# Kernel optimization log

Measured on AMD Instinct MI355X. Metric: run time of the kernel, lower is better.

Reference implementation:

```python
import jax, jax.numpy as jnp
import numpy as np

B, I, O = 128, 256, 4096
DECAY = 0.95


def setup_inputs() -> dict:
    key = jax.random.key(0)
    k_x, k_stim, k_a = jax.random.split(key, 3)
    return {
        "x": jax.random.normal(k_x, (B, I), dtype=jnp.float32),
        "stim": jax.random.normal(k_stim, (O, I), dtype=jnp.float32),
        "a": jax.random.normal(k_a, (O,), dtype=jnp.float32),
        "b": jnp.ones((O,), dtype=jnp.float32),
        "state": jnp.zeros((B, O), dtype=jnp.float32),
    }


def reference(x, stim, a, b, state):
    # L-inf distance between every input row and every stimulus row.
    # (B, 1, I) - (1, O, I) -> (B, O, I); max over input dim -> (B, O)
    distances = jnp.max(jnp.abs(x[:, None, :] - stim[None, :, :]), axis=-1)
    value = jax.nn.sigmoid((a[None, :] - distances) * b[None, :])  # (B, O)
    new_state = state * DECAY + value
    return new_state
```

## Files before the change

kernel.cpp:

```cpp
#include <hip/hip_runtime.h>
#include <math.h>

#define BB 128
#define II 256
#define OO 4096
#define DECAY 0.95f

constexpr int TB  = 16;
constexpr int TO  = 64;
constexpr int IC  = 64;
constexpr int PAD = 4;
constexpr int LDW = IC + PAD;

__global__ __launch_bounds__(256) void stimulus_linf_kernel(
    const float* __restrict__ x,
    const float* __restrict__ stim,
    const float* __restrict__ a,
    const float* __restrict__ b,
    const float* __restrict__ state,
    float* __restrict__ out)
{
    __shared__ float s_stim[TO][LDW];

    const int tid  = threadIdx.x;
    const int lane = tid & 63;
    const int wave = tid >> 6;

    const int o_tile  = blockIdx.x & 63;
    const int bi_tile = blockIdx.x >> 6;
    const int o_base  = o_tile * TO;
    const int bi_base = bi_tile * TB;

    const int wrow = __builtin_amdgcn_readfirstlane(bi_base + wave * 4);

    float d[4] = {0.f, 0.f, 0.f, 0.f};

    for (int ic = 0; ic < II; ic += IC) {
        #pragma unroll
        for (int k = 0; k < 4; ++k) {
            const int idx = tid + k * 256;
            const int row = idx >> 4;
            const int c4  = idx & 15;
            const float4 v = *reinterpret_cast<const float4*>(
                &stim[(o_base + row) * II + ic + c4 * 4]);
            *reinterpret_cast<float4*>(&s_stim[row][c4 * 4]) = v;
        }
        __syncthreads();

        const float4* xr0 = reinterpret_cast<const float4*>(x + (wrow + 0) * II + ic);
        const float4* xr1 = reinterpret_cast<const float4*>(x + (wrow + 1) * II + ic);
        const float4* xr2 = reinterpret_cast<const float4*>(x + (wrow + 2) * II + ic);
        const float4* xr3 = reinterpret_cast<const float4*>(x + (wrow + 3) * II + ic);

        #pragma unroll
        for (int i4 = 0; i4 < IC / 4; ++i4) {
            const float4 s4 =
                *reinterpret_cast<const float4*>(&s_stim[lane][i4 * 4]);
            const float4 xv0 = xr0[i4];
            const float4 xv1 = xr1[i4];
            const float4 xv2 = xr2[i4];
            const float4 xv3 = xr3[i4];
            d[0] = fmaxf(fmaxf(d[0], fabsf(xv0.x - s4.x)), fabsf(xv0.y - s4.y));
            d[0] = fmaxf(fmaxf(d[0], fabsf(xv0.z - s4.z)), fabsf(xv0.w - s4.w));
            d[1] = fmaxf(fmaxf(d[1], fabsf(xv1.x - s4.x)), fabsf(xv1.y - s4.y));
            d[1] = fmaxf(fmaxf(d[1], fabsf(xv1.z - s4.z)), fabsf(xv1.w - s4.w));
            d[2] = fmaxf(fmaxf(d[2], fabsf(xv2.x - s4.x)), fabsf(xv2.y - s4.y));
            d[2] = fmaxf(fmaxf(d[2], fabsf(xv2.z - s4.z)), fabsf(xv2.w - s4.w));
            d[3] = fmaxf(fmaxf(d[3], fabsf(xv3.x - s4.x)), fabsf(xv3.y - s4.y));
            d[3] = fmaxf(fmaxf(d[3], fabsf(xv3.z - s4.z)), fabsf(xv3.w - s4.w));
        }
        __syncthreads();
    }

    const int o  = o_base + lane;
    const float av = a[o];
    const float bv = b[o];
    #pragma unroll
    for (int r = 0; r < 4; ++r) {
        const int bi = bi_base + wave * 4 + r;
        const float z   = (av - d[r]) * bv;
        const float val = 1.f / (1.f + __expf(-z));
        out[bi * OO + o] = state[bi * OO + o] * DECAY + val;
    }
}

extern "C" void kernel_launch(void* const* d_in, const int* in_sizes, int n_in,
                              void* d_out, int out_size, void* d_ws, size_t ws_size,
                              hipStream_t stream) {
    const float* x     = (const float*)d_in[0];
    const float* stim  = (const float*)d_in[1];
    const float* a     = (const float*)d_in[2];
    const float* b     = (const float*)d_in[3];
    const float* state = (const float*)d_in[4];
    float* out = (float*)d_out;

    const dim3 grid((OO / TO) * (BB / TB));
    const dim3 block(256);
    stimulus_linf_kernel<<<grid, block, 0, stream>>>(x, stim, a, b, state, out);
}
```

Before: 78.27 us.

## Stage full stim tile in two halves, overlap second load with compute

```diff
diff --git a/kernel.cpp b/kernel.cpp
--- a/kernel.cpp
+++ b/kernel.cpp
@@ -8,9 +8,8 @@
 
 constexpr int TB  = 16;
 constexpr int TO  = 64;
-constexpr int IC  = 64;
 constexpr int PAD = 4;
-constexpr int LDW = IC + PAD;
+constexpr int LDW = II + PAD;
 
 __global__ __launch_bounds__(256) void stimulus_linf_kernel(
     const float* __restrict__ x,
@@ -33,27 +32,36 @@
 
     const int wrow = __builtin_amdgcn_readfirstlane(bi_base + wave * 4);
 
+    const int o   = o_base + lane;
+    const float av = a[o];
+    const float bv = b[o];
+    float st[4];
+    #pragma unroll
+    for (int r = 0; r < 4; ++r)
+        st[r] = state[(bi_base + wave * 4 + r) * OO + o];
+
+    const float4* xr0 = reinterpret_cast<const float4*>(x + (wrow + 0) * II);
+    const float4* xr1 = reinterpret_cast<const float4*>(x + (wrow + 1) * II);
+    const float4* xr2 = reinterpret_cast<const float4*>(x + (wrow + 2) * II);
+    const float4* xr3 = reinterpret_cast<const float4*>(x + (wrow + 3) * II);
+
     float d[4] = {0.f, 0.f, 0.f, 0.f};
 
-    for (int ic = 0; ic < II; ic += IC) {
+    auto stage = [&](int h) {
         #pragma unroll
-        for (int k = 0; k < 4; ++k) {
+        for (int k = 0; k < 8; ++k) {
             const int idx = tid + k * 256;
-            const int row = idx >> 4;
-            const int c4  = idx & 15;
+            const int row = idx >> 5;
+            const int col = h * 128 + (idx & 31) * 4;
             const float4 v = *reinterpret_cast<const float4*>(
-                &stim[(o_base + row) * II + ic + c4 * 4]);
-            *reinterpret_cast<float4*>(&s_stim[row][c4 * 4]) = v;
+                &stim[(o_base + row) * II + col]);
+            *reinterpret_cast<float4*>(&s_stim[row][col]) = v;
         }
-        __syncthreads();
+    };
 
-        const float4* xr0 = reinterpret_cast<const float4*>(x + (wrow + 0) * II + ic);
-        const float4* xr1 = reinterpret_cast<const float4*>(x + (wrow + 1) * II + ic);
-        const float4* xr2 = reinterpret_cast<const float4*>(x + (wrow + 2) * II + ic);
-        const float4* xr3 = reinterpret_cast<const float4*>(x + (wrow + 3) * II + ic);
-
-        #pragma unroll
-        for (int i4 = 0; i4 < IC / 4; ++i4) {
+    auto compute = [&](int i4lo, int i4hi) {
+        #pragma unroll 8
+        for (int i4 = i4lo; i4 < i4hi; ++i4) {
             const float4 s4 =
                 *reinterpret_cast<const float4*>(&s_stim[lane][i4 * 4]);
             const float4 xv0 = xr0[i4];
@@ -69,18 +77,21 @@
             d[3] = fmaxf(fmaxf(d[3], fabsf(xv3.x - s4.x)), fabsf(xv3.y - s4.y));
             d[3] = fmaxf(fmaxf(d[3], fabsf(xv3.z - s4.z)), fabsf(xv3.w - s4.w));
         }
-        __syncthreads();
-    }
+    };
 
-    const int o  = o_base + lane;
-    const float av = a[o];
-    const float bv = b[o];
+    stage(0);
+    __syncthreads();
+    stage(1);
+    compute(0, 32);
+    __syncthreads();
+    compute(32, 64);
+
     #pragma unroll
     for (int r = 0; r < 4; ++r) {
         const int bi = bi_base + wave * 4 + r;
         const float z   = (av - d[r]) * bv;
         const float val = 1.f / (1.f + __expf(-z));
-        out[bi * OO + o] = state[bi * OO + o] * DECAY + val;
+        out[bi * OO + o] = st[r] * DECAY + val;
     }
 }
 
```

Measured after the change: 73.26 us. 6.4% less time.
